# Performance work log

Hardware: AMD Instinct MI355X
Metric: run time of the kernel (lower is better)

## Reference

```python
import jax, jax.numpy as jnp
import numpy as np

N, M, D = 32768, 4096, 32


def setup_inputs() -> dict:
    key = jax.random.key(0)
    k1, k2, k3 = jax.random.split(key, 3)
    X = jax.random.normal(k1, (N, D), dtype=jnp.float32)
    centers = jax.random.normal(k2, (M, D), dtype=jnp.float32)
    # fitted Nystrom coefficients (params from .fit); b = Vj(1) in the Genred formula
    alphas = jax.random.normal(k3, (M, 1), dtype=jnp.float32) * 0.05
    sigma = jnp.ones((1,), dtype=jnp.float32)  # Pm(1) kernel lengthscale g
    return {"X": X, "centers": centers, "alphas": alphas, "sigma": sigma}


def reference(X, centers, alphas, sigma):
    # Genred formula: Exp(SqDist(x/g, y/g) * IntInv(-2)) * b, reduced over j (axis=1)
    g = sigma[0]
    xs = X / g           # [N, D]
    ys = centers / g     # [M, D]
    x2 = jnp.sum(xs * xs, axis=1, keepdims=True)            # [N, 1]
    y2 = jnp.sum(ys * ys, axis=1, keepdims=True).T          # [1, M]
    sqdist = x2 + y2 - 2.0 * (xs @ ys.T)                    # [N, M]
    k = jnp.exp(-0.5 * sqdist)                              # RBF kernel values
    return k @ alphas                                       # [N, 1]
```

## Files before the change

kernel.cpp:

```cpp
#include <hip/hip_runtime.h>

#define NN 32768
#define MM 4096
#define DD 32

typedef short short8 __attribute__((ext_vector_type(8)));
typedef float f32x4 __attribute__((ext_vector_type(4)));

#define ROWTILES 2
#define WAVES 4

__device__ __forceinline__ unsigned short f2bf(float f) {
    unsigned u = __float_as_uint(f);
    unsigned r = 0x7FFFu + ((u >> 16) & 1u);
    return (unsigned short)((u + r) >> 16);
}
__device__ __forceinline__ float bf2f(unsigned short h) {
    return __uint_as_float(((unsigned)h) << 16);
}

__global__ __launch_bounds__(256) void prep_kern(
    const float* __restrict__ X, const float* __restrict__ C,
    const float* __restrict__ alphas, const float* __restrict__ sigma,
    unsigned short* __restrict__ Xh, unsigned short* __restrict__ Xl,
    unsigned short* __restrict__ Ch, unsigned short* __restrict__ Cl,
    float* __restrict__ Bx, float* __restrict__ w)
{
    int i = blockIdx.x * 256 + threadIdx.x;
    float g = sigma[0];
    float LA = 1.44269504088896340736f / (g * g);

    const float* src;
    unsigned short* dh;
    unsigned short* dl;
    int row;
    bool isX = (i < NN);
    if (isX) {
        row = i;
        src = X + (size_t)row * DD;
        dh = Xh + (size_t)row * DD;
        dl = Xl + (size_t)row * DD;
    } else {
        row = i - NN;
        if (row >= MM) return;
        src = C + (size_t)row * DD;
        dh = Ch + (size_t)row * DD;
        dl = Cl + (size_t)row * DD;
    }
    const float scale = isX ? LA : 1.0f;

    float s2 = 0.f;
#pragma unroll
    for (int q = 0; q < DD / 8; ++q) {
        float4 a = ((const float4*)src)[2 * q];
        float4 b = ((const float4*)src)[2 * q + 1];
        float vv[8] = {a.x, a.y, a.z, a.w, b.x, b.y, b.z, b.w};
        short8 hv, lv;
#pragma unroll
        for (int e = 0; e < 8; ++e) {
            float v = vv[e];
            s2 = fmaf(v, v, s2);
            float sv = v * scale;
            unsigned short h = f2bf(sv);
            hv[e] = (short)h;
            lv[e] = (short)f2bf(sv - bf2f(h));
        }
        ((short8*)dh)[q] = hv;
        ((short8*)dl)[q] = lv;
    }
    float b = -0.5f * LA * s2;
    if (isX) Bx[row] = b;
    else     w[row] = alphas[row] * exp2f(b);
}

template <int MS>
__global__ __launch_bounds__(256, 8) void rbf_mfma_lds(
    const unsigned short* __restrict__ Xh, const unsigned short* __restrict__ Xl,
    const unsigned short* __restrict__ Ch, const unsigned short* __restrict__ Cl,
    const float* __restrict__ Bx, const float* __restrict__ w,
    float* __restrict__ part)
{
    constexpr int MPER = MM / MS;
    constexpr int NT = MPER / 16;
    __shared__ unsigned short sCh[MPER * DD];
    __shared__ unsigned short sCl[MPER * DD];
    __shared__ float sw[MPER];

    const int tid = threadIdx.x;
    const int wave = tid >> 6;
    const int lane = tid & 63;
    const int l15 = lane & 15;
    const int lhi = lane >> 4;
    const int rowbase = (blockIdx.x * WAVES + wave) * (16 * ROWTILES);
    const int slice = blockIdx.y;
    const int j0 = slice * MPER;

    {
        const float4* gh = (const float4*)(Ch + (size_t)j0 * DD);
        const float4* gl = (const float4*)(Cl + (size_t)j0 * DD);
        float4* lh = (float4*)sCh;
        float4* ll = (float4*)sCl;
        constexpr int NV = MPER * DD / 8;
#pragma unroll
        for (int o = tid; o < NV; o += 256) {
            lh[o] = gh[o];
            ll[o] = gl[o];
        }
        if (tid < MPER) sw[tid] = w[j0 + tid];
    }

    short8 ah[ROWTILES], al[ROWTILES];
#pragma unroll
    for (int t = 0; t < ROWTILES; ++t) {
        int r = rowbase + t * 16 + l15;
        ah[t] = *(const short8*)(Xh + (size_t)r * DD + lhi * 8);
        al[t] = *(const short8*)(Xl + (size_t)r * DD + lhi * 8);
    }
    f32x4 bx[ROWTILES];
#pragma unroll
    for (int t = 0; t < ROWTILES; ++t) {
        float4 v = *(const float4*)&Bx[rowbase + t * 16 + lhi * 4];
        bx[t][0] = v.x; bx[t][1] = v.y; bx[t][2] = v.z; bx[t][3] = v.w;
    }

    f32x4 acc[ROWTILES];
#pragma unroll
    for (int t = 0; t < ROWTILES; ++t) acc[t] = (f32x4){0.f, 0.f, 0.f, 0.f};

    __syncthreads();

#pragma unroll 2
    for (int jt = 0; jt < NT; ++jt) {
        const int r = jt * 16 + l15;
        short8 bh = *(const short8*)&sCh[r * DD + lhi * 8];
        short8 bl = *(const short8*)&sCl[r * DD + lhi * 8];
        float wj = sw[r];
#pragma unroll
        for (int t = 0; t < ROWTILES; ++t) {
            f32x4 d = bx[t];
            d = __builtin_amdgcn_mfma_f32_16x16x32_bf16(ah[t], bl, d, 0, 0, 0);
            d = __builtin_amdgcn_mfma_f32_16x16x32_bf16(al[t], bh, d, 0, 0, 0);
            d = __builtin_amdgcn_mfma_f32_16x16x32_bf16(ah[t], bh, d, 0, 0, 0);
#pragma unroll
            for (int rr = 0; rr < 4; ++rr)
                acc[t][rr] = fmaf(wj, __builtin_amdgcn_exp2f(d[rr]), acc[t][rr]);
        }
    }

#pragma unroll
    for (int t = 0; t < ROWTILES; ++t)
#pragma unroll
        for (int rr = 0; rr < 4; ++rr) {
            float v = acc[t][rr];
            v += __shfl_xor(v, 1, 64);
            v += __shfl_xor(v, 2, 64);
            v += __shfl_xor(v, 4, 64);
            v += __shfl_xor(v, 8, 64);
            acc[t][rr] = v;
        }
    if (l15 == 0) {
#pragma unroll
        for (int t = 0; t < ROWTILES; ++t)
            *(f32x4*)&part[(size_t)slice * NN + rowbase + t * 16 + lhi * 4] = acc[t];
    }
}

template <int MS>
__global__ __launch_bounds__(256) void reduce_kern(const float* __restrict__ part,
                                                   float* __restrict__ out) {
    int i = blockIdx.x * 256 + threadIdx.x;
    float s = 0.f;
#pragma unroll
    for (int k = 0; k < MS; ++k) s += part[(size_t)k * NN + i];
    out[i] = s;
}

__global__ __launch_bounds__(256) void wkern(const float* __restrict__ C,
                                             const float* __restrict__ alphas,
                                             const float* __restrict__ sigma,
                                             float* __restrict__ w) {
    int j = blockIdx.x * 256 + threadIdx.x;
    if (j >= MM) return;
    float g = sigma[0];
    float inv_g2 = 1.0f / (g * g);
    const float4* cp = (const float4*)(C + (size_t)j * DD);
    float y2 = 0.f;
#pragma unroll
    for (int q = 0; q < DD / 4; ++q) {
        float4 v = cp[q];
        y2 = fmaf(v.x, v.x, y2);
        y2 = fmaf(v.y, v.y, y2);
        y2 = fmaf(v.z, v.z, y2);
        y2 = fmaf(v.w, v.w, y2);
    }
    w[j] = alphas[j] * exp2f(-0.5f * inv_g2 * 1.44269504088896340736f * y2);
}

__global__ __launch_bounds__(128) void rbf_valu(const float* __restrict__ X,
                                                const float* __restrict__ C,
                                                const float* __restrict__ w,
                                                const float* __restrict__ sigma,
                                                float* __restrict__ out) {
    const int row = blockIdx.x * 128 + threadIdx.x;
    const float g = sigma[0];
    const float A = 1.44269504088896340736f / (g * g);
    float x[DD];
    const float4* xp = (const float4*)(X + (size_t)row * DD);
#pragma unroll
    for (int q = 0; q < DD / 4; ++q) {
        float4 v = xp[q];
        x[4 * q + 0] = v.x; x[4 * q + 1] = v.y;
        x[4 * q + 2] = v.z; x[4 * q + 3] = v.w;
    }
    float x2 = 0.f;
#pragma unroll
    for (int d = 0; d < DD; ++d) x2 = fmaf(x[d], x[d], x2);
    const float B = -0.5f * A * x2;
    float acc = 0.f;
#pragma unroll 2
    for (int j = 0; j < MM; ++j) {
        const float* cj = C + (size_t)j * DD;
        float d0 = 0.f, d1 = 0.f, d2 = 0.f, d3 = 0.f;
#pragma unroll
        for (int d = 0; d < DD; d += 4) {
            d0 = fmaf(cj[d + 0], x[d + 0], d0);
            d1 = fmaf(cj[d + 1], x[d + 1], d1);
            d2 = fmaf(cj[d + 2], x[d + 2], d2);
            d3 = fmaf(cj[d + 3], x[d + 3], d3);
        }
        float dot = (d0 + d1) + (d2 + d3);
        acc = fmaf(w[j], exp2f(fmaf(dot, A, B)), acc);
    }
    out[row] = acc;
}

extern "C" void kernel_launch(void* const* d_in, const int* in_sizes, int n_in,
                              void* d_out, int out_size, void* d_ws, size_t ws_size,
                              hipStream_t stream) {
    const float* X  = (const float*)d_in[0];
    const float* C  = (const float*)d_in[1];
    const float* al = (const float*)d_in[2];
    const float* sg = (const float*)d_in[3];
    float* out = (float*)d_out;

    size_t off = 0;
    unsigned short* Xh = (unsigned short*)((char*)d_ws + off); off += (size_t)NN * DD * 2;
    unsigned short* Xl = (unsigned short*)((char*)d_ws + off); off += (size_t)NN * DD * 2;
    unsigned short* Ch = (unsigned short*)((char*)d_ws + off); off += (size_t)MM * DD * 2;
    unsigned short* Cl = (unsigned short*)((char*)d_ws + off); off += (size_t)MM * DD * 2;
    float* Bx = (float*)((char*)d_ws + off); off += (size_t)NN * 4;
    float* w  = (float*)((char*)d_ws + off); off += (size_t)MM * 4;
    float* part = (float*)((char*)d_ws + off);
    const size_t base = off;

    const size_t need32 = base + (size_t)32 * NN * 4;
    const size_t need8  = base + (size_t)8 * NN * 4;

    if (ws_size >= need8) {
        prep_kern<<<(NN + MM) / 256, 256, 0, stream>>>(X, C, al, sg, Xh, Xl, Ch, Cl, Bx, w);
        if (ws_size >= need32) {
            dim3 grid(NN / (WAVES * 16 * ROWTILES), 32);
            rbf_mfma_lds<32><<<grid, 64 * WAVES, 0, stream>>>(Xh, Xl, Ch, Cl, Bx, w, part);
            reduce_kern<32><<<NN / 256, 256, 0, stream>>>(part, out);
        } else {
            dim3 grid(NN / (WAVES * 16 * ROWTILES), 8);
            rbf_mfma_lds<8><<<grid, 64 * WAVES, 0, stream>>>(Xh, Xl, Ch, Cl, Bx, w, part);
            reduce_kern<8><<<NN / 256, 256, 0, stream>>>(part, out);
        }
    } else {
        float* wf = (float*)d_ws;
        wkern<<<MM / 256, 256, 0, stream>>>(C, al, sg, wf);
        rbf_valu<<<NN / 128, 128, 0, stream>>>(X, C, wf, sg, out);
    }
}
```

Measured before the change: 42.56 us.

## Double row tiles per wave, interleave MFMA chains, parallelize prep across four threads per row

```diff
diff --git a/kernel.cpp b/kernel.cpp
--- a/kernel.cpp
+++ b/kernel.cpp
@@ -7,7 +7,7 @@
 typedef short short8 __attribute__((ext_vector_type(8)));
 typedef float f32x4 __attribute__((ext_vector_type(4)));
 
-#define ROWTILES 2
+#define ROWTILES 4
 #define WAVES 4
 
 __device__ __forceinline__ unsigned short f2bf(float f) {
@@ -26,55 +26,47 @@
     unsigned short* __restrict__ Ch, unsigned short* __restrict__ Cl,
     float* __restrict__ Bx, float* __restrict__ w)
 {
-    int i = blockIdx.x * 256 + threadIdx.x;
-    float g = sigma[0];
-    float LA = 1.44269504088896340736f / (g * g);
-
-    const float* src;
-    unsigned short* dh;
-    unsigned short* dl;
-    int row;
-    bool isX = (i < NN);
-    if (isX) {
-        row = i;
-        src = X + (size_t)row * DD;
-        dh = Xh + (size_t)row * DD;
-        dl = Xl + (size_t)row * DD;
-    } else {
-        row = i - NN;
-        if (row >= MM) return;
-        src = C + (size_t)row * DD;
-        dh = Ch + (size_t)row * DD;
-        dl = Cl + (size_t)row * DD;
-    }
+    const int i = blockIdx.x * 256 + threadIdx.x;
+    const int row = i >> 2;
+    const int q = i & 3;
+    const float g = sigma[0];
+    const float LA = 1.44269504088896340736f / (g * g);
+
+    const bool isX = (row < NN);
+    const int crow = isX ? row : (row - NN);
+    const float* src = (isX ? X + (size_t)row * DD : C + (size_t)crow * DD) + q * 8;
+    unsigned short* dh = (isX ? Xh + (size_t)row * DD : Ch + (size_t)crow * DD) + q * 8;
+    unsigned short* dl = (isX ? Xl + (size_t)row * DD : Cl + (size_t)crow * DD) + q * 8;
     const float scale = isX ? LA : 1.0f;
 
+    float4 a = ((const float4*)src)[0];
+    float4 b = ((const float4*)src)[1];
+    float vv[8] = {a.x, a.y, a.z, a.w, b.x, b.y, b.z, b.w};
     float s2 = 0.f;
-#pragma unroll
-    for (int q = 0; q < DD / 8; ++q) {
-        float4 a = ((const float4*)src)[2 * q];
-        float4 b = ((const float4*)src)[2 * q + 1];
-        float vv[8] = {a.x, a.y, a.z, a.w, b.x, b.y, b.z, b.w};
-        short8 hv, lv;
-#pragma unroll
-        for (int e = 0; e < 8; ++e) {
-            float v = vv[e];
-            s2 = fmaf(v, v, s2);
-            float sv = v * scale;
-            unsigned short h = f2bf(sv);
-            hv[e] = (short)h;
-            lv[e] = (short)f2bf(sv - bf2f(h));
-        }
-        ((short8*)dh)[q] = hv;
-        ((short8*)dl)[q] = lv;
-    }
-    float b = -0.5f * LA * s2;
-    if (isX) Bx[row] = b;
-    else     w[row] = alphas[row] * exp2f(b);
+    short8 hv, lv;
+#pragma unroll
+    for (int e = 0; e < 8; ++e) {
+        float v = vv[e];
+        s2 = fmaf(v, v, s2);
+        float sv = v * scale;
+        unsigned short h = f2bf(sv);
+        hv[e] = (short)h;
+        lv[e] = (short)f2bf(sv - bf2f(h));
+    }
+    *(short8*)dh = hv;
+    *(short8*)dl = lv;
+
+    s2 += __shfl_xor(s2, 1, 64);
+    s2 += __shfl_xor(s2, 2, 64);
+    if (q == 0) {
+        float bb = -0.5f * LA * s2;
+        if (isX) Bx[row] = bb;
+        else     w[crow] = alphas[crow] * exp2f(bb);
+    }
 }
 
 template <int MS>
-__global__ __launch_bounds__(256, 8) void rbf_mfma_lds(
+__global__ __launch_bounds__(256, 4) void rbf_mfma_lds(
     const unsigned short* __restrict__ Xh, const unsigned short* __restrict__ Xl,
     const unsigned short* __restrict__ Ch, const unsigned short* __restrict__ Cl,
     const float* __restrict__ Bx, const float* __restrict__ w,
@@ -95,16 +87,17 @@
     const int slice = blockIdx.y;
     const int j0 = slice * MPER;
 
+    const char* lh = (const char*)sCh;
+    const char* ll = (const char*)sCl;
+
     {
         const float4* gh = (const float4*)(Ch + (size_t)j0 * DD);
         const float4* gl = (const float4*)(Cl + (size_t)j0 * DD);
-        float4* lh = (float4*)sCh;
-        float4* ll = (float4*)sCl;
         constexpr int NV = MPER * DD / 8;
 #pragma unroll
         for (int o = tid; o < NV; o += 256) {
-            lh[o] = gh[o];
-            ll[o] = gl[o];
+            ((float4*)sCh)[o] = gh[o];
+            ((float4*)sCl)[o] = gl[o];
         }
         if (tid < MPER) sw[tid] = w[j0 + tid];
     }
@@ -129,22 +122,28 @@
 
     __syncthreads();
 
-#pragma unroll 2
+    const int lbase = l15 * 64 + lhi * 16;
+
+#pragma unroll
     for (int jt = 0; jt < NT; ++jt) {
-        const int r = jt * 16 + l15;
-        short8 bh = *(const short8*)&sCh[r * DD + lhi * 8];
-        short8 bl = *(const short8*)&sCl[r * DD + lhi * 8];
-        float wj = sw[r];
-#pragma unroll
-        for (int t = 0; t < ROWTILES; ++t) {
-            f32x4 d = bx[t];
-            d = __builtin_amdgcn_mfma_f32_16x16x32_bf16(ah[t], bl, d, 0, 0, 0);
-            d = __builtin_amdgcn_mfma_f32_16x16x32_bf16(al[t], bh, d, 0, 0, 0);
-            d = __builtin_amdgcn_mfma_f32_16x16x32_bf16(ah[t], bh, d, 0, 0, 0);
+        short8 bh = *(const short8*)(lh + lbase + jt * 1024);
+        short8 bl = *(const short8*)(ll + lbase + jt * 1024);
+        float wj = sw[jt * 16 + l15];
+        f32x4 d[ROWTILES];
+#pragma unroll
+        for (int t = 0; t < ROWTILES; ++t)
+            d[t] = __builtin_amdgcn_mfma_f32_16x16x32_bf16(ah[t], bl, bx[t], 0, 0, 0);
+#pragma unroll
+        for (int t = 0; t < ROWTILES; ++t)
+            d[t] = __builtin_amdgcn_mfma_f32_16x16x32_bf16(al[t], bh, d[t], 0, 0, 0);
+#pragma unroll
+        for (int t = 0; t < ROWTILES; ++t)
+            d[t] = __builtin_amdgcn_mfma_f32_16x16x32_bf16(ah[t], bh, d[t], 0, 0, 0);
+#pragma unroll
+        for (int t = 0; t < ROWTILES; ++t)
 #pragma unroll
             for (int rr = 0; rr < 4; ++rr)
-                acc[t][rr] = fmaf(wj, __builtin_amdgcn_exp2f(d[rr]), acc[t][rr]);
-        }
+                acc[t][rr] = fmaf(wj, __builtin_amdgcn_exp2f(d[t][rr]), acc[t][rr]);
     }
 
 #pragma unroll
@@ -257,7 +256,7 @@
     const size_t need8  = base + (size_t)8 * NN * 4;
 
     if (ws_size >= need8) {
-        prep_kern<<<(NN + MM) / 256, 256, 0, stream>>>(X, C, al, sg, Xh, Xl, Ch, Cl, Bx, w);
+        prep_kern<<<(NN + MM) * 4 / 256, 256, 0, stream>>>(X, C, al, sg, Xh, Xl, Ch, Cl, Bx, w);
         if (ws_size >= need32) {
             dim3 grid(NN / (WAVES * 16 * ROWTILES), 32);
             rbf_mfma_lds<32><<<grid, 64 * WAVES, 0, stream>>>(Xh, Xl, Ch, Cl, Bx, w, part);
```

After: 99.24 us. +133.2%, slower.
